# Performance work log

Hardware: AMD Instinct MI355X
Metric: run time of the kernel (lower is better)

## Reference

```python
import jax, jax.numpy as jnp
import numpy as np

N_NODES = 50000
N_EDGES = 1600000
D_IN = 128
D_HID = 128
D_OUT = 128


def setup_inputs() -> dict:
    key = jax.random.key(0)
    k1, k2, k3, k4, k5, k6 = jax.random.split(key, 6)
    x = jax.random.normal(k1, (N_NODES, D_IN), dtype=jnp.float32)
    edge_index = jax.random.randint(k2, (2, N_EDGES), 0, N_NODES, dtype=jnp.int64)
    # glorot-ish init for GCNConv linear weights; bias zeros-like but randomized small
    W1 = jax.random.normal(k3, (D_IN, D_HID), dtype=jnp.float32) * (1.0 / np.sqrt(D_IN))
    b1 = jax.random.normal(k4, (D_HID,), dtype=jnp.float32) * 0.01
    W2 = jax.random.normal(k5, (D_HID, D_OUT), dtype=jnp.float32) * (1.0 / np.sqrt(D_HID))
    b2 = jax.random.normal(k6, (D_OUT,), dtype=jnp.float32) * 0.01
    return {"x": x, "edge_index": edge_index, "W1": W1, "b1": b1, "W2": W2, "b2": b2}


def gcn_conv(x, src, dst, W, b, n_nodes):
    # PyG GCNConv: add self-loops, symmetric normalization deg^-1/2, lin -> aggregate -> +bias
    loop = jnp.arange(n_nodes, dtype=src.dtype)
    s = jnp.concatenate([src, loop])  # [E+N]
    d = jnp.concatenate([dst, loop])  # [E+N]
    deg = jax.ops.segment_sum(jnp.ones_like(d, dtype=x.dtype), d, num_segments=n_nodes)
    dinv = jnp.where(deg > 0, jax.lax.rsqrt(deg), 0.0)
    norm = dinv[s] * dinv[d]  # [E+N]
    h = x @ W  # [N, F_out]
    msg = h[s] * norm[:, None]  # gather + scale: [E+N, F_out]
    out = jax.ops.segment_sum(msg, d, num_segments=n_nodes)  # scatter-add
    return out + b


def reference(x, edge_index, W1, b1, W2, b2):
    src, dst = edge_index[0], edge_index[1]
    h = gcn_conv(x, src, dst, W1, b1, N_NODES)
    h = jnp.where(h >= 0, h, 0.1 * h)  # LeakyReLU(0.1)
    h = gcn_conv(h, src, dst, W2, b2, N_NODES)
    return h.mean(axis=1)  # [N]
```

## Files before the change

### kernel.cpp

```cpp
#include <hip/hip_runtime.h>
#include <hip/hip_bf16.h>


#define N_NODES 50000
#define NPAD 50048
#define D 128
#define BK 196
#define CHUNK 4096

typedef unsigned int uint;
typedef unsigned short u16;
typedef __attribute__((ext_vector_type(8))) short short8;
typedef __attribute__((ext_vector_type(4))) float floatx4;

__device__ __forceinline__ u16 cvt_bf16(float f) {
    uint u = __float_as_uint(f);
    return (u16)((u + 0x7fffu + ((u >> 16) & 1u)) >> 16);
}
__device__ __forceinline__ uint pack_bf2(float a, float b) {
    return (uint)cvt_bf16(a) | ((uint)cvt_bf16(b) << 16);
}

__global__ void hist_w2m_kernel(const int* __restrict__ dst, uint* __restrict__ H,
                                const float* __restrict__ W2, const float* __restrict__ b2,
                                float* __restrict__ w2m, uint* __restrict__ counter,
                                int E, int CHN) {
    int t = threadIdx.x, c = blockIdx.x;
    if (c < CHN) {
        __shared__ uint h[BK];
        if (t < BK) h[t] = 0;
        __syncthreads();
        int e0 = c * CHUNK;
        for (int i = t; i < CHUNK; i += 256) {
            int e = e0 + i;
            if (e < E) atomicAdd(&h[dst[e] >> 8], 1u);
        }
        __syncthreads();
        if (t < BK) H[t * CHN + c] = h[t];
    } else {
        if (t < 128) {
            float s = 0.f;
            for (int j = 0; j < 128; j++) s += W2[t * 128 + j];
            w2m[t] = s * (1.0f / 128.0f);
        } else if (t == 128) {
            float s = 0.f;
            for (int j = 0; j < 128; j++) s += b2[j];
            w2m[128] = s * (1.0f / 128.0f);
        } else if (t == 129) {
            *counter = 0;
        }
    }
}

__global__ void scan_kernel(uint* __restrict__ H, uint* __restrict__ T, uint* __restrict__ B,
                            int* __restrict__ row, uint* __restrict__ counter,
                            int CHN, int E, int N) {
    __shared__ uint s[256];
    __shared__ uint ticket_sh;
    int t = threadIdx.x, b = blockIdx.x;
    uint carry = 0;
    for (int base = 0; base < CHN; base += 256) {
        int idx = base + t;
        uint v = (idx < CHN) ? H[b * CHN + idx] : 0u;
        s[t] = v;
        __syncthreads();
#pragma unroll
        for (int off = 1; off < 256; off <<= 1) {
            uint u = (t >= off) ? s[t - off] : 0u;
            __syncthreads();
            s[t] += u;
            __syncthreads();
        }
        if (idx < CHN) H[b * CHN + idx] = carry + s[t] - v;
        carry += s[255];
        __syncthreads();
    }
    if (t == 0) {
        atomicExch(&T[b], carry);
        __threadfence();
        ticket_sh = atomicAdd(counter, 1);
    }
    __syncthreads();
    if (ticket_sh == (uint)(gridDim.x - 1)) {
        __threadfence();
        uint v = (t < BK) ? atomicAdd(&T[t], 0u) : 0u;
        s[t] = v;
        __syncthreads();
#pragma unroll
        for (int off = 1; off < 256; off <<= 1) {
            uint u = (t >= off) ? s[t - off] : 0u;
            __syncthreads();
            s[t] += u;
            __syncthreads();
        }
        if (t < BK) B[t] = s[t] - v;
        if (t == 0) { B[BK] = (uint)E; row[N] = E; }
    }
}

__global__ void scatter_kernel(const int* __restrict__ src, const int* __restrict__ dst,
                               const uint* __restrict__ H, const uint* __restrict__ B,
                               uint* __restrict__ EB, int E, int CHN) {
    __shared__ uint cur[BK];
    int t = threadIdx.x, c = blockIdx.x;
    if (t < BK) cur[t] = B[t] + H[t * CHN + c];
    __syncthreads();
    int e0 = c * CHUNK;
    for (int i = t; i < CHUNK; i += 256) {
        int e = e0 + i;
        if (e < E) {
            int d = dst[e];
            uint slot = atomicAdd(&cur[d >> 8], 1u);
            EB[slot] = ((uint)(d & 255) << 16) | (uint)src[e];
        }
    }
}

#define WT_STRIDE 136
union SortGemmSmem {
    struct { uint cnt[256], s[256], cur[256]; } sort;
    u16 wt[128 * WT_STRIDE];
};
__global__ __launch_bounds__(256) void sortgemm_kernel(
    const uint* __restrict__ EB, const uint* __restrict__ B,
    int* __restrict__ row, float* __restrict__ dinv, u16* __restrict__ esrc,
    const float* __restrict__ A, const float* __restrict__ W,
    uint* __restrict__ G32, int N, int M) {
    __shared__ SortGemmSmem sm;
    int t = threadIdx.x;

    if (blockIdx.x < BK) {
        int b = blockIdx.x;
        uint base = B[b], ne = B[b + 1] - base;
        sm.sort.cnt[t] = 0;
        __syncthreads();
        for (uint i = t; i < ne; i += 256) atomicAdd(&sm.sort.cnt[EB[base + i] >> 16], 1u);
        __syncthreads();
        uint c = sm.sort.cnt[t];
        sm.sort.s[t] = c;
        __syncthreads();
#pragma unroll
        for (int off = 1; off < 256; off <<= 1) {
            uint u = (t >= off) ? sm.sort.s[t - off] : 0u;
            __syncthreads();
            sm.sort.s[t] += u;
            __syncthreads();
        }
        uint p = sm.sort.s[t] - c;
        int v = (b << 8) + t;
        if (v < N) {
            row[v] = (int)(base + p);
            dinv[v] = rsqrtf((float)(c + 1u));
        }
        sm.sort.cur[t] = base + p;
        __syncthreads();
        for (uint i = t; i < ne; i += 256) {
            uint u = EB[base + i];
            uint slot = atomicAdd(&sm.sort.cur[u >> 16], 1u);
            esrc[slot] = (u16)(u & 0xffffu);
        }
    } else {
        int bid = blockIdx.x - BK;
        for (int i = t; i < 128 * 128; i += 256) {
            int k = i >> 7, n = i & 127;
            sm.wt[n * WT_STRIDE + k] = cvt_bf16(W[i]);
        }
        __syncthreads();

        int wave = t >> 6, lane = t & 63;
        int m = lane & 15, quad = lane >> 4;
        int rowa = bid * 64 + wave * 16 + m;
        int rowc = rowa < M ? rowa : M - 1;
        const float* Arow = A + (long)rowc * D;

        short8 afrag[4];
#pragma unroll
        for (int kt = 0; kt < 4; kt++) {
            int k0 = kt * 32 + quad * 8;
            float4 f0 = *(const float4*)(Arow + k0);
            float4 f1 = *(const float4*)(Arow + k0 + 4);
            short8 af;
            af[0] = (short)cvt_bf16(f0.x); af[1] = (short)cvt_bf16(f0.y);
            af[2] = (short)cvt_bf16(f0.z); af[3] = (short)cvt_bf16(f0.w);
            af[4] = (short)cvt_bf16(f1.x); af[5] = (short)cvt_bf16(f1.y);
            af[6] = (short)cvt_bf16(f1.z); af[7] = (short)cvt_bf16(f1.w);
            afrag[kt] = af;
        }

        int orow0 = bid * 64 + wave * 16;
        for (int n0 = 0; n0 < 128; n0 += 16) {
            floatx4 acc = {0.f, 0.f, 0.f, 0.f};
#pragma unroll
            for (int kt = 0; kt < 4; kt++) {
                short8 bf = *(const short8*)(sm.wt + (n0 + m) * WT_STRIDE + kt * 32 + quad * 8);
                acc = __builtin_amdgcn_mfma_f32_16x16x32_bf16(afrag[kt], bf, acc, 0, 0, 0);
            }
#pragma unroll
            for (int r = 0; r < 4; r++) {
                float val = acc[r];
                float oth = __shfl_xor(val, 1, 64);
                int orow = orow0 + quad * 4 + r;
                if (orow < M && (m & 1) == 0)
                    G32[(long)orow * 64 + ((n0 + m) >> 1)] = pack_bf2(val, oth);
            }
        }
    }
}

__global__ __launch_bounds__(256) void gather_node_kernel(
    const int* __restrict__ row, const u16* __restrict__ esrc,
    const uint* __restrict__ g16, const float* __restrict__ dinv,
    const float* __restrict__ b1, const float* __restrict__ w2m,
    float* __restrict__ mg, int N) {
    int wave = threadIdx.x >> 6;
    int lane = threadIdx.x & 63;
    int sub = lane & 7;
    int nb = lane >> 3;
    int v = blockIdx.x * 4 + wave;
    if (v >= N) return;

    const uint4* gv = (const uint4*)g16;
    float dvv = dinv[v];
    float acc[16];
#pragma unroll
    for (int i = 0; i < 16; i++) acc[i] = 0.f;

#define ACC8(ua, ub, wgt) {                                              \
    uint uu[8] = {(ua).x, (ua).y, (ua).z, (ua).w, (ub).x, (ub).y, (ub).z, (ub).w}; \
    _Pragma("unroll")                                                    \
    for (int i = 0; i < 8; i++) {                                        \
        acc[2*i]   += (wgt) * __uint_as_float(uu[i] << 16);              \
        acc[2*i+1] += (wgt) * __uint_as_float(uu[i] & 0xffff0000u);      \
    } }

    if (nb == 0) {
        long rb = (long)v * 16 + 2 * sub;
        uint4 ua = gv[rb], ub = gv[rb + 1];
        ACC8(ua, ub, dvv)
    }
    int jb = row[v], je = row[v + 1];
    int j = jb + nb;
    if (j < je) {
        int s0 = esrc[j];
        float wA = dinv[s0];
        long r0 = (long)s0 * 16 + 2 * sub;
        uint4 p0 = gv[r0], p1 = gv[r0 + 1];
        j += 8;
        while (j < je) {
            int s1 = esrc[j];
            float wB = dinv[s1];
            long r1 = (long)s1 * 16 + 2 * sub;
            uint4 q0 = gv[r1], q1 = gv[r1 + 1];
            j += 8;
            ACC8(p0, p1, wA)
            p0 = q0; p1 = q1; wA = wB;
        }
        ACC8(p0, p1, wA)
    }
#undef ACC8

#pragma unroll
    for (int i = 0; i < 16; i++) {
        acc[i] += __shfl_xor(acc[i], 8, 64);
        acc[i] += __shfl_xor(acc[i], 16, 64);
        acc[i] += __shfl_xor(acc[i], 32, 64);
    }

    if (nb == 0) {
        const float4* bp = (const float4*)b1;
        const float4* wp = (const float4*)w2m;
        float s = 0.f;
#pragma unroll
        for (int q4 = 0; q4 < 4; q4++) {
            float4 bb = bp[sub * 4 + q4];
            float4 wm = wp[sub * 4 + q4];
            float t0 = dvv * acc[4*q4 + 0] + bb.x; t0 = t0 >= 0.f ? t0 : 0.1f * t0;
            float t1 = dvv * acc[4*q4 + 1] + bb.y; t1 = t1 >= 0.f ? t1 : 0.1f * t1;
            float t2 = dvv * acc[4*q4 + 2] + bb.z; t2 = t2 >= 0.f ? t2 : 0.1f * t2;
            float t3 = dvv * acc[4*q4 + 3] + bb.w; t3 = t3 >= 0.f ? t3 : 0.1f * t3;
            s += t0 * wm.x + t1 * wm.y + t2 * wm.z + t3 * wm.w;
        }
        s += __shfl_xor(s, 1, 64);
        s += __shfl_xor(s, 2, 64);
        s += __shfl_xor(s, 4, 64);
        if (sub == 0) mg[v] = dvv * s;
    }
}

__global__ void out_kernel(const int* __restrict__ row, const u16* __restrict__ esrc,
                           const float* __restrict__ mg, const float* __restrict__ dinv,
                           const float* __restrict__ w2m, float* __restrict__ out, int N) {
    int v = blockIdx.x * blockDim.x + threadIdx.x;
    if (v >= N) return;
    float acc = mg[v];
    int jb = row[v], je = row[v + 1];
    int j = jb;
    for (; j + 8 <= je; j += 8) {
        acc += mg[esrc[j]] + mg[esrc[j + 1]] + mg[esrc[j + 2]] + mg[esrc[j + 3]] +
               mg[esrc[j + 4]] + mg[esrc[j + 5]] + mg[esrc[j + 6]] + mg[esrc[j + 7]];
    }
    for (; j < je; j++) acc += mg[esrc[j]];
    out[v] = dinv[v] * acc + w2m[128];
}

extern "C" void kernel_launch(void* const* d_in, const int* in_sizes, int n_in,
                              void* d_out, int out_size, void* d_ws, size_t ws_size,
                              hipStream_t stream) {
    const float* x  = (const float*)d_in[0];
    const int* ei   = (const int*)d_in[1];
    const float* W1 = (const float*)d_in[2];
    const float* b1 = (const float*)d_in[3];
    const float* W2 = (const float*)d_in[4];
    const float* b2 = (const float*)d_in[5];
    float* out = (float*)d_out;

    const int N = N_NODES;
    const int E = in_sizes[1] / 2;
    const int* src = ei;
    const int* dst = ei + E;
    const int CHN = (E + CHUNK - 1) / CHUNK;
    const int nblocks = (N + 255) / 256;

    float*    dinv    = (float*)d_ws;
    int*      row     = (int*)(dinv + NPAD);
    uint*     B       = (uint*)(row + NPAD + 16);
    float*    w2m     = (float*)(B + 256);
    float*    mg      = w2m + 256;
    uint*     T       = (uint*)(mg + NPAD);
    uint*     counter = T + 256;
    uint*     g16u    = counter + 16;
    u16*      esrc    = (u16*)(g16u + (long)NPAD * 64);
    uint*     H       = (uint*)(esrc + E);
    uint*     EB      = H + BK * CHN;

    hist_w2m_kernel<<<CHN + 1, 256, 0, stream>>>(dst, H, W2, b2, w2m, counter, E, CHN);
    scan_kernel<<<BK, 256, 0, stream>>>(H, T, B, row, counter, CHN, E, N);
    scatter_kernel<<<CHN, 256, 0, stream>>>(src, dst, H, B, EB, E, CHN);
    sortgemm_kernel<<<BK + (N + 63) / 64, 256, 0, stream>>>(EB, B, row, dinv, esrc,
                                                            x, W1, g16u, N, N);
    gather_node_kernel<<<(N + 3) / 4, 256, 0, stream>>>(row, esrc, g16u, dinv, b1, w2m, mg, N);
    out_kernel<<<nblocks, 256, 0, stream>>>(row, esrc, mg, dinv, w2m, out, N);
}
```

Measured before the change: 196.1 us.

## Split hidden features into column quarters for cache-local gather with partial sums

The GEMM output is now written column-blocked, as four 32-column slabs of bf16 features, instead of full 256-byte rows. The gather kernel processes one slab per block, interleaved so neighbouring blocks share a node range. This shrinks each gathered slab's working set to fit better in L2/MALL. Each slab produces a partial dot product with w2m, and a new small kernel sums the four partials and applies dinv. The costs are an extra kernel launch, four re-reads of the CSR edge list, and partial-sum traffic.

```diff
diff --git a/kernel.cpp b/kernel.cpp
--- a/kernel.cpp
+++ b/kernel.cpp
@@ -200,91 +200,100 @@
                 float val = acc[r];
                 float oth = __shfl_xor(val, 1, 64);
                 int orow = orow0 + quad * 4 + r;
-                if (orow < M && (m & 1) == 0)
-                    G32[(long)orow * 64 + ((n0 + m) >> 1)] = pack_bf2(val, oth);
+                if (orow < M && (m & 1) == 0) {
+                    int c = n0 + m;
+                    G32[(long)(c >> 5) * NPAD * 16 + (long)orow * 16 + ((c & 31) >> 1)]
+                        = pack_bf2(val, oth);
+                }
             }
         }
     }
 }
 
-__global__ __launch_bounds__(256) void gather_node_kernel(
+__global__ __launch_bounds__(256) void gather_q2_kernel(
     const int* __restrict__ row, const u16* __restrict__ esrc,
     const uint* __restrict__ g16, const float* __restrict__ dinv,
     const float* __restrict__ b1, const float* __restrict__ w2m,
-    float* __restrict__ mg, int N) {
+    float* __restrict__ partial, int N) {
+    int b = blockIdx.x;
+    int slot = b & 7;
+    int q = slot >> 1;
     int wave = threadIdx.x >> 6;
     int lane = threadIdx.x & 63;
-    int sub = lane & 7;
-    int nb = lane >> 3;
-    int v = blockIdx.x * 4 + wave;
+    int grp = lane >> 4;
+    int g = lane & 15;
+    int chain = g >> 2, p = g & 3;
+    int v = (b >> 3) * 32 + (slot & 1) * 16 + wave * 4 + grp;
     if (v >= N) return;
 
-    const uint4* gv = (const uint4*)g16;
+    const uint4* gq = (const uint4*)(g16 + (long)q * NPAD * 16);
     float dvv = dinv[v];
-    float acc[16];
-#pragma unroll
-    for (int i = 0; i < 16; i++) acc[i] = 0.f;
-
-#define ACC8(ua, ub, wgt) {                                              \
-    uint uu[8] = {(ua).x, (ua).y, (ua).z, (ua).w, (ub).x, (ub).y, (ub).z, (ub).w}; \
-    _Pragma("unroll")                                                    \
-    for (int i = 0; i < 8; i++) {                                        \
-        acc[2*i]   += (wgt) * __uint_as_float(uu[i] << 16);              \
-        acc[2*i+1] += (wgt) * __uint_as_float(uu[i] & 0xffff0000u);      \
-    } }
-
-    if (nb == 0) {
-        long rb = (long)v * 16 + 2 * sub;
-        uint4 ua = gv[rb], ub = gv[rb + 1];
-        ACC8(ua, ub, dvv)
-    }
-    int jb = row[v], je = row[v + 1];
-    int j = jb + nb;
+    float acc[8];
+#pragma unroll
+    for (int i = 0; i < 8; i++) acc[i] = 0.f;
+
+#define ACC4(u, wgt) {                                                   \
+    acc[0] += (wgt) * __uint_as_float((u).x << 16);                      \
+    acc[1] += (wgt) * __uint_as_float((u).x & 0xffff0000u);              \
+    acc[2] += (wgt) * __uint_as_float((u).y << 16);                      \
+    acc[3] += (wgt) * __uint_as_float((u).y & 0xffff0000u);              \
+    acc[4] += (wgt) * __uint_as_float((u).z << 16);                      \
+    acc[5] += (wgt) * __uint_as_float((u).z & 0xffff0000u);              \
+    acc[6] += (wgt) * __uint_as_float((u).w << 16);                      \
+    acc[7] += (wgt) * __uint_as_float((u).w & 0xffff0000u); }
+
+    if (chain == 0) {
+        uint4 u = gq[(long)v * 4 + p];
+        ACC4(u, dvv)
+    }
+    int jb = (int)__builtin_nontemporal_load(&row[v]);
+    int je = (int)__builtin_nontemporal_load(&row[v + 1]);
+    int j = jb + chain;
     if (j < je) {
-        int s0 = esrc[j];
-        float wA = dinv[s0];
-        long r0 = (long)s0 * 16 + 2 * sub;
-        uint4 p0 = gv[r0], p1 = gv[r0 + 1];
-        j += 8;
+        int s0 = (int)__builtin_nontemporal_load(&esrc[j]);
+        float w0 = dinv[s0];
+        uint4 u0 = gq[(long)s0 * 4 + p];
+        j += 4;
         while (j < je) {
-            int s1 = esrc[j];
-            float wB = dinv[s1];
-            long r1 = (long)s1 * 16 + 2 * sub;
-            uint4 q0 = gv[r1], q1 = gv[r1 + 1];
-            j += 8;
-            ACC8(p0, p1, wA)
-            p0 = q0; p1 = q1; wA = wB;
-        }
-        ACC8(p0, p1, wA)
-    }
-#undef ACC8
-
-#pragma unroll
-    for (int i = 0; i < 16; i++) {
+            int s1 = (int)__builtin_nontemporal_load(&esrc[j]);
+            float w1 = dinv[s1];
+            uint4 u1 = gq[(long)s1 * 4 + p];
+            j += 4;
+            ACC4(u0, w0)
+            u0 = u1; w0 = w1;
+        }
+        ACC4(u0, w0)
+    }
+#undef ACC4
+
+#pragma unroll
+    for (int i = 0; i < 8; i++) {
+        acc[i] += __shfl_xor(acc[i], 4, 64);
         acc[i] += __shfl_xor(acc[i], 8, 64);
-        acc[i] += __shfl_xor(acc[i], 16, 64);
-        acc[i] += __shfl_xor(acc[i], 32, 64);
-    }
-
-    if (nb == 0) {
-        const float4* bp = (const float4*)b1;
-        const float4* wp = (const float4*)w2m;
-        float s = 0.f;
-#pragma unroll
-        for (int q4 = 0; q4 < 4; q4++) {
-            float4 bb = bp[sub * 4 + q4];
-            float4 wm = wp[sub * 4 + q4];
-            float t0 = dvv * acc[4*q4 + 0] + bb.x; t0 = t0 >= 0.f ? t0 : 0.1f * t0;
-            float t1 = dvv * acc[4*q4 + 1] + bb.y; t1 = t1 >= 0.f ? t1 : 0.1f * t1;
-            float t2 = dvv * acc[4*q4 + 2] + bb.z; t2 = t2 >= 0.f ? t2 : 0.1f * t2;
-            float t3 = dvv * acc[4*q4 + 3] + bb.w; t3 = t3 >= 0.f ? t3 : 0.1f * t3;
-            s += t0 * wm.x + t1 * wm.y + t2 * wm.z + t3 * wm.w;
-        }
-        s += __shfl_xor(s, 1, 64);
-        s += __shfl_xor(s, 2, 64);
-        s += __shfl_xor(s, 4, 64);
-        if (sub == 0) mg[v] = dvv * s;
-    }
+    }
+
+    const float2* bp = (const float2*)b1;
+    const float2* wp = (const float2*)w2m;
+    float s = 0.f;
+#pragma unroll
+    for (int k = 0; k < 4; k++) {
+        float2 bb = bp[q * 16 + p * 4 + k];
+        float2 wm = wp[q * 16 + p * 4 + k];
+        float t0 = dvv * acc[2 * k]     + bb.x; t0 = t0 >= 0.f ? t0 : 0.1f * t0;
+        float t1 = dvv * acc[2 * k + 1] + bb.y; t1 = t1 >= 0.f ? t1 : 0.1f * t1;
+        s += t0 * wm.x + t1 * wm.y;
+    }
+    s += __shfl_xor(s, 1, 64);
+    s += __shfl_xor(s, 2, 64);
+    if (g == 0) partial[q * NPAD + v] = s;
+}
+
+__global__ void mg_kernel(const float* __restrict__ partial, const float* __restrict__ dinv,
+                          float* __restrict__ mg, int N) {
+    int v = blockIdx.x * blockDim.x + threadIdx.x;
+    if (v >= N) return;
+    mg[v] = dinv[v] * (partial[v] + partial[NPAD + v] +
+                       partial[2 * NPAD + v] + partial[3 * NPAD + v]);
 }
 
 __global__ void out_kernel(const int* __restrict__ row, const u16* __restrict__ esrc,
@@ -328,7 +337,8 @@
     float*    mg      = w2m + 256;
     uint*     T       = (uint*)(mg + NPAD);
     uint*     counter = T + 256;
-    uint*     g16u    = counter + 16;
+    float*    partial = (float*)(counter + 16);
+    uint*     g16u    = (uint*)(partial + 4 * NPAD);
     u16*      esrc    = (u16*)(g16u + (long)NPAD * 64);
     uint*     H       = (uint*)(esrc + E);
     uint*     EB      = H + BK * CHN;
@@ -338,6 +348,8 @@
     scatter_kernel<<<CHN, 256, 0, stream>>>(src, dst, H, B, EB, E, CHN);
     sortgemm_kernel<<<BK + (N + 63) / 64, 256, 0, stream>>>(EB, B, row, dinv, esrc,
                                                             x, W1, g16u, N, N);
-    gather_node_kernel<<<(N + 3) / 4, 256, 0, stream>>>(row, esrc, g16u, dinv, b1, w2m, mg, N);
+    gather_q2_kernel<<<((N + 31) / 32) * 8, 256, 0, stream>>>(row, esrc, g16u, dinv,
+                                                              b1, w2m, partial, N);
+    mg_kernel<<<nblocks, 256, 0, stream>>>(partial, dinv, mg, N);
     out_kernel<<<nblocks, 256, 0, stream>>>(row, esrc, mg, dinv, w2m, out, N);
 }
```

Result: slower. 228.8 us (+16.7%).
